# Kernel optimization log

Measured on AMD Instinct MI355X. Metric: run time of the kernel, lower is better.

## Reference

```python
import jax, jax.numpy as jnp
import numpy as np

N = 8192       # nodes == in_channels (diff matrix is NxN)
DF = 256       # feature dim of z
E = 65536      # edges (unused by forward, kept for signature fidelity)
M = 4096       # len(reliable_negatives)
NEG = 10       # neg_samples
STEPS = 10     # num_diffusion_steps
TEMP = 0.2


def setup_inputs() -> dict:
    key = jax.random.key(0)
    k1, k2, k3, k4, k5 = jax.random.split(key, 5)
    z = jax.random.normal(k1, (N, DF), dtype=jnp.float32)
    # learned parameter; init positive-uniform so row sums are well conditioned
    diff_matrix = jax.random.uniform(k2, (N, N), dtype=jnp.float32)
    edge_index = jax.random.randint(k3, (2, E), 0, N)
    reliable_negatives = jax.random.randint(k4, (M,), 0, N)
    # deterministic stand-in for torch.randint(0, len(reliable_negatives), (neg_samples,))
    neg_idx = jax.random.randint(k5, (NEG,), 0, M)
    return {"z": z, "diff_matrix": diff_matrix, "edge_index": edge_index,
            "reliable_negatives": reliable_negatives, "neg_idx": neg_idx}


def _l2norm(x):
    # F.normalize(dim=1): divide by L2 norm clamped at 1e-12
    n = jnp.sqrt(jnp.sum(x * x, axis=1, keepdims=True))
    return x / jnp.maximum(n, 1e-12)


def reference(z, diff_matrix, edge_index, reliable_negatives, neg_idx):
    # 10-step loop: mm(inverse(diag(rowsum)), M) == row-wise reciprocal scaling
    dm = diff_matrix
    for _ in range(STEPS):
        dm = dm / jnp.sum(dm, axis=1, keepdims=True)  # [N, N]
    # (normalized_diff_matrix with +eps*I is computed in the original but unused)

    anchor = z                       # [N, DF]
    positive = dm @ z                # [N, DF] diffused features
    negative = z[neg_idx]            # [NEG, DF]

    a = _l2norm(anchor)
    p = _l2norm(positive)
    n = _l2norm(negative)

    pos_sim = jnp.sum(a * p, axis=1) / TEMP                 # [N]
    neg_sim = jnp.exp(jnp.einsum('nd,kd->nk', a, n) / TEMP)  # [N, NEG]
    loss = -jnp.log(jnp.exp(pos_sim) / (jnp.exp(pos_sim) + neg_sim.sum(axis=1))).mean()
    return loss
```

## Files before the change

### kernel.cpp

```cpp
#include <hip/hip_runtime.h>
#include <hip/hip_bf16.h>


typedef float f32x4 __attribute__((ext_vector_type(4)));
typedef short s16x8 __attribute__((ext_vector_type(8)));

#define NN 8192
#define DFF 256
#define NNEG 10

__device__ __forceinline__ unsigned short f2bf(float x) {
  return __builtin_bit_cast(unsigned short, __float2bfloat16(x));
}

__device__ __forceinline__ void gload_lds16(const void* g, void* l) {
  __builtin_amdgcn_global_load_lds(
      (const __attribute__((address_space(1))) void*)(void*)g,
      (__attribute__((address_space(3))) void*)l, 16, 0, 0);
}

__device__ __forceinline__ float dot4(float4 a, float4 b) {
  return a.x * b.x + a.y * b.y + a.z * b.z + a.w * b.w;
}

__global__ void k_transpose(const float* __restrict__ z,
                            unsigned short* __restrict__ zT) {
  __shared__ float tile[64][65];
  const int bx = blockIdx.x;
  const int by = blockIdx.y;
  const int t = threadIdx.x;
  const int lc = t & 63, lq = t >> 6;
#pragma unroll
  for (int p = 0; p < 16; ++p) {
    const int lr = lq * 16 + p;
    tile[lr][lc] = z[(size_t)(bx * 64 + lr) * DFF + by * 64 + lc];
  }
  __syncthreads();
#pragma unroll
  for (int p = 0; p < 16; ++p) {
    const int tc = lq * 16 + p;
    zT[(size_t)(by * 64 + tc) * NN + bx * 64 + lc] = f2bf(tile[lc][tc]);
  }
}

__global__ __launch_bounds__(256, 2) void k_gemm(const float* __restrict__ dm,
                                                 const unsigned short* __restrict__ zT,
                                                 float* __restrict__ part, int KS) {
  __shared__ unsigned short sA[2][64 * 64];
  __shared__ unsigned short sB[2][256 * 64];
  const int bx = blockIdx.x;
  const int mtile = bx & 127;
  const int ks = bx >> 7;
  const int klen = NN / KS;
  const int k0 = ks * klen;
  const int steps = klen / 64;
  const int tid = threadIdx.x;
  const int w = tid >> 6;
  const int l = tid & 63;
  const int m0 = mtile * 64;

  f32x4 acc[4][4] = {};

  const int ar = tid >> 4;
  const int ac = (tid & 15) * 4;

  const int rq = l >> 3;
  const int bsw = (l & 7) * 16;
  const int blog = bsw ^ (rq << 4);

  float4 areg[4];

#define LOAD_A(kt)                                                             \
  _Pragma("unroll") for (int p = 0; p < 4; ++p) areg[p] =                      \
      *(const float4*)(dm + (size_t)(m0 + p * 16 + ar) * NN + k0 + (kt)*64 + ac);

#define WRITE_A(buf)                                                           \
  _Pragma("unroll") for (int p = 0; p < 4; ++p) {                              \
    const int r = p * 16 + ar;                                                 \
    ushort4 h;                                                                 \
    h.x = f2bf(areg[p].x); h.y = f2bf(areg[p].y);                              \
    h.z = f2bf(areg[p].z); h.w = f2bf(areg[p].w);                              \
    *(ushort4*)&sA[buf][r * 64 + (ac ^ ((r & 7) << 3))] = h;                   \
  }

#define STAGE_B(kt, buf)                                                       \
  {                                                                            \
    const char* srcbase = (const char*)zT + (size_t)(k0 + (kt)*64) * 2 + blog; \
    _Pragma("unroll") for (int q = 0; q < 8; ++q) {                            \
      gload_lds16(srcbase + (size_t)(w * 64 + q * 8 + rq) * (NN * 2),          \
                  (char*)sB[buf] + (w * 64 + q * 8) * 128);                    \
    }                                                                          \
  }

  STAGE_B(0, 0);
  LOAD_A(0);
  WRITE_A(0);
  __syncthreads();

  for (int kt = 0; kt < steps; ++kt) {
    const int cur = kt & 1, nxt = cur ^ 1;
    if (kt + 1 < steps) {
      LOAD_A(kt + 1);
      STAGE_B(kt + 1, nxt);
    }
#pragma unroll
    for (int kc = 0; kc < 2; ++kc) {
      const int e = kc * 32 + (l >> 4) * 8;
      s16x8 af[4], bfr[4];
#pragma unroll
      for (int mi = 0; mi < 4; ++mi) {
        const int r = mi * 16 + (l & 15);
        af[mi] = *(const s16x8*)&sA[cur][r * 64 + (e ^ ((r & 7) << 3))];
      }
#pragma unroll
      for (int nj = 0; nj < 4; ++nj) {
        const int rn = w * 64 + nj * 16 + (l & 15);
        bfr[nj] = *(const s16x8*)&sB[cur][rn * 64 + (e ^ ((rn & 7) << 3))];
      }
#pragma unroll
      for (int mi = 0; mi < 4; ++mi)
#pragma unroll
        for (int nj = 0; nj < 4; ++nj)
          acc[mi][nj] = __builtin_amdgcn_mfma_f32_16x16x32_bf16(
              af[mi], bfr[nj], acc[mi][nj], 0, 0, 0);
    }
    if (kt + 1 < steps) {
      WRITE_A(nxt);
    }
    __syncthreads();
  }

  float* cb = part + (size_t)ks * NN * DFF;
#pragma unroll
  for (int mi = 0; mi < 4; ++mi)
#pragma unroll
    for (int nj = 0; nj < 4; ++nj) {
      const int col = w * 64 + nj * 16 + (l & 15);
      const int row0 = m0 + mi * 16 + (l >> 4) * 4;
#pragma unroll
      for (int r = 0; r < 4; ++r)
        cb[(size_t)(row0 + r) * DFF + col] = acc[mi][nj][r];
    }
#undef LOAD_A
#undef WRITE_A
#undef STAGE_B
}

__global__ __launch_bounds__(256) void k_loss(const float* __restrict__ z,
                                              const float* __restrict__ part,
                                              const int* __restrict__ neg_idx,
                                              float* __restrict__ lpart, int KS) {
  __shared__ float sneg[NNEG * DFF];
  __shared__ float swsum[4];
  const int t = threadIdx.x;
  const int w = t >> 6, l = t & 63;
  for (int k = w; k < NNEG; k += 4) {
    const int idx = neg_idx[k];
    float4 v = *(const float4*)(z + (size_t)idx * DFF + l * 4);
    float ss = dot4(v, v);
#pragma unroll
    for (int off = 32; off > 0; off >>= 1) ss += __shfl_xor(ss, off);
    const float s = 1.0f / fmaxf(sqrtf(ss), 1e-12f);
    float4 o;
    o.x = v.x * s; o.y = v.y * s; o.z = v.z * s; o.w = v.w * s;
    *(float4*)&sneg[k * DFF + l * 4] = o;
  }
  __syncthreads();
  const int gw = blockIdx.x * 4 + w;
  float lsum = 0.f;
  for (int rr = 0; rr < 8; ++rr) {
    const int i = gw * 8 + rr;
    const float4 a = *(const float4*)(z + (size_t)i * DFF + l * 4);
    float4 p; p.x = 0.f; p.y = 0.f; p.z = 0.f; p.w = 0.f;
    for (int ksp = 0; ksp < KS; ++ksp) {
      const float4 q = *(const float4*)(part + ((size_t)ksp * NN + i) * DFF + l * 4);
      p.x += q.x; p.y += q.y; p.z += q.z; p.w += q.w;
    }
    float vals[13];
    vals[0] = dot4(a, a);
    vals[1] = dot4(p, p);
    vals[2] = dot4(a, p);
#pragma unroll
    for (int k = 0; k < NNEG; ++k) {
      const float4 nv = *(const float4*)&sneg[k * DFF + l * 4];
      vals[3 + k] = dot4(a, nv);
    }
#pragma unroll
    for (int off = 32; off > 0; off >>= 1)
#pragma unroll
      for (int j = 0; j < 13; ++j) vals[j] += __shfl_xor(vals[j], off);
    const float na = fmaxf(sqrtf(vals[0]), 1e-12f);
    const float npp = fmaxf(sqrtf(vals[1]), 1e-12f);
    const float ps = vals[2] / (na * npp) * 5.0f;
    float S = 0.f;
#pragma unroll
    for (int k = 0; k < NNEG; ++k) S += expf(vals[3 + k] / na * 5.0f);
    lsum += logf(expf(ps) + S) - ps;
  }
  if (l == 0) swsum[w] = lsum;
  __syncthreads();
  if (t == 0) lpart[blockIdx.x] = swsum[0] + swsum[1] + swsum[2] + swsum[3];
}

__global__ void k_final(const float* __restrict__ lpart, float* __restrict__ out) {
  const int t = threadIdx.x;
  float v = lpart[t] + lpart[t + 64] + lpart[t + 128] + lpart[t + 192];
#pragma unroll
  for (int off = 32; off > 0; off >>= 1) v += __shfl_xor(v, off);
  if (t == 0) out[0] = v * (1.0f / (float)NN);
}

extern "C" void kernel_launch(void* const* d_in, const int* in_sizes, int n_in,
                              void* d_out, int out_size, void* d_ws, size_t ws_size,
                              hipStream_t stream) {
  const float* z = (const float*)d_in[0];
  const float* dm = (const float*)d_in[1];
  const int* neg_idx = (const int*)d_in[4];
  float* out = (float*)d_out;

  auto need = [](size_t ks) {
    return (size_t)4 * 1024 * 1024 + ks * (size_t)NN * DFF * 4 + 1024;
  };
  int KS = 4;
  if (ws_size < need(4)) KS = (ws_size >= need(2)) ? 2 : 1;

  char* ws = (char*)d_ws;
  unsigned short* zT = (unsigned short*)ws;
  float* part = (float*)(ws + (size_t)4 * 1024 * 1024);
  float* lpart = (float*)(ws + (size_t)4 * 1024 * 1024 + (size_t)KS * NN * DFF * 4);

  k_transpose<<<dim3(128, 4), 256, 0, stream>>>(z, zT);
  k_gemm<<<128 * KS, 256, 0, stream>>>(dm, zT, part, KS);
  k_loss<<<256, 256, 0, stream>>>(z, part, neg_idx, lpart, KS);
  k_final<<<1, 64, 0, stream>>>(lpart, out);
}
```

Baseline: 124.7 us.

## Load GEMM operands directly into registers, bypassing LDS staging

The GEMM kernel drops its shared-memory double buffers and barriers. Each wave now loads its A (fp32 diff matrix) and B (bf16 transposed z) MFMA fragments straight from global memory into registers, converting A to bf16 in registers. A two-deep register ping-pong prefetch with a k-step of 32 tries to hide load latency. The cost is that all four waves in a block fetch the same A rows redundantly, and each lane's 32-byte row segments may coalesce poorly.

```diff
diff --git a/kernel.cpp b/kernel.cpp
--- a/kernel.cpp
+++ b/kernel.cpp
@@ -11,12 +11,6 @@
 
 __device__ __forceinline__ unsigned short f2bf(float x) {
   return __builtin_bit_cast(unsigned short, __float2bfloat16(x));
-}
-
-__device__ __forceinline__ void gload_lds16(const void* g, void* l) {
-  __builtin_amdgcn_global_load_lds(
-      (const __attribute__((address_space(1))) void*)(void*)g,
-      (__attribute__((address_space(3))) void*)l, 16, 0, 0);
 }
 
 __device__ __forceinline__ float dot4(float4 a, float4 b) {
@@ -46,89 +40,84 @@
 __global__ __launch_bounds__(256, 2) void k_gemm(const float* __restrict__ dm,
                                                  const unsigned short* __restrict__ zT,
                                                  float* __restrict__ part, int KS) {
-  __shared__ unsigned short sA[2][64 * 64];
-  __shared__ unsigned short sB[2][256 * 64];
   const int bx = blockIdx.x;
   const int mtile = bx & 127;
   const int ks = bx >> 7;
   const int klen = NN / KS;
   const int k0 = ks * klen;
-  const int steps = klen / 64;
+  const int steps = klen / 32;
   const int tid = threadIdx.x;
   const int w = tid >> 6;
   const int l = tid & 63;
   const int m0 = mtile * 64;
+  const int lr = l & 15;
+  const int kl = (l >> 4) * 8;
+
+  const float* pa[4];
+  const unsigned short* pb[4];
+#pragma unroll
+  for (int mi = 0; mi < 4; ++mi)
+    pa[mi] = dm + (size_t)(m0 + mi * 16 + lr) * NN + kl;
+#pragma unroll
+  for (int nj = 0; nj < 4; ++nj)
+    pb[nj] = zT + (size_t)(w * 64 + nj * 16 + lr) * NN + kl;
 
   f32x4 acc[4][4] = {};
-
-  const int ar = tid >> 4;
-  const int ac = (tid & 15) * 4;
-
-  const int rq = l >> 3;
-  const int bsw = (l & 7) * 16;
-  const int blog = bsw ^ (rq << 4);
-
-  float4 areg[4];
-
-#define LOAD_A(kt)                                                             \
-  _Pragma("unroll") for (int p = 0; p < 4; ++p) areg[p] =                      \
-      *(const float4*)(dm + (size_t)(m0 + p * 16 + ar) * NN + k0 + (kt)*64 + ac);
-
-#define WRITE_A(buf)                                                           \
-  _Pragma("unroll") for (int p = 0; p < 4; ++p) {                              \
-    const int r = p * 16 + ar;                                                 \
-    ushort4 h;                                                                 \
-    h.x = f2bf(areg[p].x); h.y = f2bf(areg[p].y);                              \
-    h.z = f2bf(areg[p].z); h.w = f2bf(areg[p].w);                              \
-    *(ushort4*)&sA[buf][r * 64 + (ac ^ ((r & 7) << 3))] = h;                   \
-  }
-
-#define STAGE_B(kt, buf)                                                       \
+  float4 Fa[4][2], Fb[4][2];
+  s16x8 Aa[4], Ab[4], Ba[4], Bb[4];
+
+#define KBOF(kt) (k0 + ((kt) < steps ? (kt) : steps - 1) * 32)
+
+#define LOADA(kt, F)                                                           \
   {                                                                            \
-    const char* srcbase = (const char*)zT + (size_t)(k0 + (kt)*64) * 2 + blog; \
-    _Pragma("unroll") for (int q = 0; q < 8; ++q) {                            \
-      gload_lds16(srcbase + (size_t)(w * 64 + q * 8 + rq) * (NN * 2),          \
-                  (char*)sB[buf] + (w * 64 + q * 8) * 128);                    \
+    const int kb_ = KBOF(kt);                                                  \
+    _Pragma("unroll") for (int mi = 0; mi < 4; ++mi) {                         \
+      F[mi][0] = *(const float4*)(pa[mi] + kb_);                               \
+      F[mi][1] = *(const float4*)(pa[mi] + kb_ + 4);                           \
     }                                                                          \
   }
 
-  STAGE_B(0, 0);
-  LOAD_A(0);
-  WRITE_A(0);
-  __syncthreads();
-
-  for (int kt = 0; kt < steps; ++kt) {
-    const int cur = kt & 1, nxt = cur ^ 1;
-    if (kt + 1 < steps) {
-      LOAD_A(kt + 1);
-      STAGE_B(kt + 1, nxt);
-    }
-#pragma unroll
-    for (int kc = 0; kc < 2; ++kc) {
-      const int e = kc * 32 + (l >> 4) * 8;
-      s16x8 af[4], bfr[4];
-#pragma unroll
-      for (int mi = 0; mi < 4; ++mi) {
-        const int r = mi * 16 + (l & 15);
-        af[mi] = *(const s16x8*)&sA[cur][r * 64 + (e ^ ((r & 7) << 3))];
-      }
-#pragma unroll
-      for (int nj = 0; nj < 4; ++nj) {
-        const int rn = w * 64 + nj * 16 + (l & 15);
-        bfr[nj] = *(const s16x8*)&sB[cur][rn * 64 + (e ^ ((rn & 7) << 3))];
-      }
-#pragma unroll
-      for (int mi = 0; mi < 4; ++mi)
-#pragma unroll
-        for (int nj = 0; nj < 4; ++nj)
-          acc[mi][nj] = __builtin_amdgcn_mfma_f32_16x16x32_bf16(
-              af[mi], bfr[nj], acc[mi][nj], 0, 0, 0);
-    }
-    if (kt + 1 < steps) {
-      WRITE_A(nxt);
-    }
-    __syncthreads();
-  }
+#define LOADB(kt, Bf)                                                          \
+  {                                                                            \
+    const int kb_ = KBOF(kt);                                                  \
+    _Pragma("unroll") for (int nj = 0; nj < 4; ++nj) Bf[nj] =                  \
+        *(const s16x8*)(pb[nj] + kb_);                                         \
+  }
+
+#define CVTA(F, Af)                                                            \
+  _Pragma("unroll") for (int mi = 0; mi < 4; ++mi) {                           \
+    s16x8 t_;                                                                  \
+    t_[0] = (short)f2bf(F[mi][0].x); t_[1] = (short)f2bf(F[mi][0].y);          \
+    t_[2] = (short)f2bf(F[mi][0].z); t_[3] = (short)f2bf(F[mi][0].w);          \
+    t_[4] = (short)f2bf(F[mi][1].x); t_[5] = (short)f2bf(F[mi][1].y);          \
+    t_[6] = (short)f2bf(F[mi][1].z); t_[7] = (short)f2bf(F[mi][1].w);          \
+    Af[mi] = t_;                                                               \
+  }
+
+#define MFMAS(Af, Bf)                                                          \
+  _Pragma("unroll") for (int mi = 0; mi < 4; ++mi)                             \
+      _Pragma("unroll") for (int nj = 0; nj < 4; ++nj) acc[mi][nj] =           \
+          __builtin_amdgcn_mfma_f32_16x16x32_bf16(Af[mi], Bf[nj],              \
+                                                  acc[mi][nj], 0, 0, 0);
+
+  LOADA(0, Fa); LOADB(0, Ba);
+  LOADA(1, Fb); LOADB(1, Bb);
+  CVTA(Fa, Aa);
+
+  for (int kt = 0; kt < steps; kt += 2) {
+    MFMAS(Aa, Ba);
+    LOADA(kt + 2, Fa); LOADB(kt + 2, Ba);
+    CVTA(Fb, Ab);
+    MFMAS(Ab, Bb);
+    LOADA(kt + 3, Fb); LOADB(kt + 3, Bb);
+    CVTA(Fa, Aa);
+  }
+
+#undef KBOF
+#undef LOADA
+#undef LOADB
+#undef CVTA
+#undef MFMAS
 
   float* cb = part + (size_t)ks * NN * DFF;
 #pragma unroll
@@ -141,9 +130,6 @@
       for (int r = 0; r < 4; ++r)
         cb[(size_t)(row0 + r) * DFF + col] = acc[mi][nj][r];
     }
-#undef LOAD_A
-#undef WRITE_A
-#undef STAGE_B
 }
 
 __global__ __launch_bounds__(256) void k_loss(const float* __restrict__ z,
```

Result: slower. 228.0 us (+82.9%).
